# Optimization experiments

Measured on AMD Instinct MI355X. Metric: run time of the kernel, lower is better.

Reference implementation:

```python
import jax, jax.numpy as jnp
import numpy as np

A = 2
IMG_C = 3
IMG_H = 64
IMG_W = 96
N_OBJ = 5   # OBJS + STACKS with REMOVE_BG
B = 64
P = 4       # number of predicate nets
CONV_OUT = 32


def setup_inputs() -> dict:
    key = jax.random.key(0)
    k0, k1, k2, k3 = jax.random.split(key, 4)
    state = jax.random.normal(k0, (B, N_OBJ, IMG_C, IMG_H, IMG_W), jnp.float32)
    state_next = jax.random.normal(k1, (B, N_OBJ, IMG_C, IMG_H, IMG_W), jnp.float32)
    # uniform object count (structural max N=5) so tuple count is static
    n_obj = jnp.full((B,), N_OBJ, dtype=jnp.int32)
    temp = jnp.float32(0.5)
    # stacked params for the P predicate nets (conv + linear head)
    conv_w = jax.random.normal(k2, (P * CONV_OUT, A * IMG_C, 3, 3), jnp.float32) * 0.05
    conv_b = jnp.zeros((P * CONV_OUT,), jnp.float32)
    w2 = jax.random.normal(k3, (P, CONV_OUT), jnp.float32) * 0.1
    b2 = jnp.zeros((P,), jnp.float32)
    return {"state": state, "state_next": state_next, "conv_w": conv_w,
            "conv_b": conv_b, "w2": w2, "b2": b2, "n_obj": n_obj, "temp": temp}


def _build_tuples(s, n):
    # cartesian_prod(arange(n), arange(n)) -> ordered pairs (i, j)
    ii = jnp.repeat(jnp.arange(n), n)   # [n*n]
    jj = jnp.tile(jnp.arange(n), n)     # [n*n]
    a = s[:, ii]                        # [B, n*n, C, H, W]
    b = s[:, jj]
    t = jnp.concatenate([a, b], axis=2)             # [B, n*n, A*C, H, W]
    return t.reshape(-1, A * IMG_C, IMG_H, IMG_W)   # [B*n*n, 6, H, W]


def _predicates(t, conv_w, conv_b, w2, b2, temp):
    # fused conv over all P nets (stacked output channels)
    y = jax.lax.conv_general_dilated(
        t, conv_w, window_strides=(2, 2), padding='SAME',
        dimension_numbers=('NCHW', 'OIHW', 'NCHW'))
    y = jax.nn.relu(y + conv_b[None, :, None, None])
    y = y.mean(axis=(2, 3)).reshape(-1, P, CONV_OUT)   # [T, P, 32]
    logits = jnp.einsum('tpc,pc->tp', y, w2) + b2      # [T, P]
    return jax.nn.sigmoid(logits / temp)


def reference(state, state_next, conv_w, conv_b, w2, b2, n_obj, temp):
    n = N_OBJ  # uniform ragged case: all n_obj entries equal the max
    tuples = _build_tuples(state, n)
    tuples_next = _build_tuples(state_next, n)
    preds = _predicates(tuples, conv_w, conv_b, w2, b2, temp)
    preds_next = _predicates(tuples_next, conv_w, conv_b, w2, b2, temp)
    # adjacency: column per tuple, one-hot in the owning sample's row
    T = B * n * n
    adj = (jnp.arange(T)[None, :] // (n * n) == jnp.arange(B)[:, None]).astype(jnp.float32)
    return preds, preds_next, adj
```

## Files before the change

### kernel.cpp

```cpp
#include <hip/hip_runtime.h>
#include <math.h>

#define BQ 64
#define NOBJ 5
#define CIN 3
#define IMG_H 64
#define IMG_W 96
#define OH 32
#define OW 48
#define NPAIR 25
#define PP 4
#define CONV_OUT 32

#define NRG 16
#define NPOS 96
#define XK 32
#define X_U32 (NOBJ * NPOS * XK / 2)
#define X_UNITS (NOBJ * NPOS * 4)

#define NPRED (2 * 1600 * PP)
#define ADJ_N (BQ * 1600)

typedef __fp16   h2 __attribute__((ext_vector_type(2)));
typedef _Float16 half8 __attribute__((ext_vector_type(8)));
typedef float    float4_ __attribute__((ext_vector_type(4)));
typedef unsigned int uint4_ __attribute__((ext_vector_type(4)));

__global__ __launch_bounds__(512) void conv_pair_mfma(
    const float* __restrict__ state,
    const float* __restrict__ state_next,
    const float* __restrict__ conv_w,
    const float* __restrict__ conv_b,
    const float* __restrict__ w2,
    float* __restrict__ T,
    float* __restrict__ out)
{
    __shared__ __align__(16) unsigned int sX32[X_U32];

    const int tid = threadIdx.x;
    const int rg  = blockIdx.x;
    const int b   = blockIdx.y;
    const int src = blockIdx.z;

    const float* g = (src == 0 ? state : state_next)
                   + (size_t)b * NOBJ * CIN * IMG_H * IMG_W;
    const int R0 = rg * 4;

    if (src == 1 && tid < 100) {
        int a  = (rg + NRG * b) * 100 + tid;
        int bb = a / 1600;
        int t  = a - bb * 1600;
        out[NPRED + a] = (t / NPAIR == bb) ? 1.0f : 0.0f;
    }

    const int wave = tid >> 6;
    const int lane = tid & 63;
    const int quad = lane >> 4;
    const int ocl  = lane & 15;

    const int mt  = wave;
    const int p   = mt >> 1;
    const int row = mt * 16 + ocl;

    half8 wa, wb;
    #pragma unroll
    for (int j = 0; j < 8; ++j) {
        int k = quad * 8 + j;
        float va = 0.f, vb = 0.f;
        if (k < 27) {
            va = conv_w[row * 54 + k];
            vb = conv_w[row * 54 + 27 + k];
        } else if (k == 27) {
            va = conv_b[row];
        }
        wa[j] = (_Float16)va;
        wb[j] = (_Float16)vb;
    }
    h2 w2h01, w2h23;
    {
        const float* wp = w2 + p * CONV_OUT + (mt & 1) * 16 + quad * 4;
        w2h01 = __builtin_amdgcn_cvt_pkrtz(wp[0], wp[1]);
        w2h23 = __builtin_amdgcn_cvt_pkrtz(wp[2], wp[3]);
    }

    {
        const int subk = tid & 3;
        int koff[8], khv[8], kwv[8];
        float padf[8];
        bool kval[8];
        #pragma unroll
        for (int j = 0; j < 8; ++j) {
            int k = subk * 8 + j;
            if (k < 27) {
                int ci = k / 9;
                int r9 = k - ci * 9;
                int kh = r9 / 3;
                int kw = r9 - kh * 3;
                koff[j] = ci * (IMG_H * IMG_W) + kh * IMG_W + kw;
                khv[j] = kh; kwv[j] = kw; kval[j] = true; padf[j] = 0.f;
            } else {
                koff[j] = 0; khv[j] = 0; kwv[j] = 0; kval[j] = false;
                padf[j] = (k == 27) ? 1.0f : 0.f;
            }
        }
        for (int u = tid; u < X_UNITS; u += 512) {
            int pl  = (u >> 2) % NPOS;
            int obj = u / (NPOS * 4);
            int rl  = (pl >= 48) ? 1 : 0;
            int pc  = pl - rl * 48;
            int gr0 = R0 + 2 * rl;
            int gc0 = 2 * pc;
            const float* gp = g + obj * (CIN * IMG_H * IMG_W) + gr0 * IMG_W + gc0;
            float fv[8];
            #pragma unroll
            for (int j = 0; j < 8; ++j) {
                float v = padf[j];
                if (kval[j] && (gr0 + khv[j] < IMG_H) && (gc0 + kwv[j] < IMG_W))
                    v = gp[koff[j]];
                fv[j] = v;
            }
            uint4_ w4;
            w4.x = __builtin_bit_cast(unsigned int, __builtin_amdgcn_cvt_pkrtz(fv[0], fv[1]));
            w4.y = __builtin_bit_cast(unsigned int, __builtin_amdgcn_cvt_pkrtz(fv[2], fv[3]));
            w4.z = __builtin_bit_cast(unsigned int, __builtin_amdgcn_cvt_pkrtz(fv[4], fv[5]));
            w4.w = __builtin_bit_cast(unsigned int, __builtin_amdgcn_cvt_pkrtz(fv[6], fv[7]));
            *(uint4_*)&sX32[(size_t)u * 4] = w4;
        }
    }

    __syncthreads();

    const float4_ zero4 = {0.f, 0.f, 0.f, 0.f};
    const h2 hz = {(__fp16)0.f, (__fp16)0.f};

    float acc[NPAIR];
    #pragma unroll
    for (int q = 0; q < NPAIR; ++q) acc[q] = 0.f;

    #pragma unroll
    for (int nt = 0; nt < 6; ++nt) {
        const int rl  = nt / 3;
        const int c0  = (nt - rl * 3) * 16;
        const int pos = rl * 48 + c0 + ocl;

        half8 xf[NOBJ];
        h2 ah01[NOBJ], ah23[NOBJ];
        #pragma unroll
        for (int obj = 0; obj < NOBJ; ++obj) {
            xf[obj] = *(const half8*)&sX32[((size_t)(obj * NPOS + pos)) * 16 + quad * 4];
            float4_ a = __builtin_amdgcn_mfma_f32_16x16x32_f16(wa, xf[obj], zero4, 0, 0, 0);
            ah01[obj] = __builtin_amdgcn_cvt_pkrtz(a[0], a[1]);
            ah23[obj] = __builtin_amdgcn_cvt_pkrtz(a[2], a[3]);
        }

        #pragma unroll
        for (int jo = 0; jo < NOBJ; ++jo) {
            float4_ bq = __builtin_amdgcn_mfma_f32_16x16x32_f16(wb, xf[jo], zero4, 0, 0, 0);
            h2 bh01 = __builtin_amdgcn_cvt_pkrtz(bq[0], bq[1]);
            h2 bh23 = __builtin_amdgcn_cvt_pkrtz(bq[2], bq[3]);
            #pragma unroll
            for (int i = 0; i < NOBJ; ++i) {
                h2 s0 = ah01[i] + bh01;
                h2 s1 = ah23[i] + bh23;
                s0 = __builtin_elementwise_max(s0, hz);
                s1 = __builtin_elementwise_max(s1, hz);
                float t0 = __builtin_amdgcn_fdot2(s0, w2h01, acc[i * NOBJ + jo], false);
                acc[i * NOBJ + jo] = __builtin_amdgcn_fdot2(s1, w2h23, t0, false);
            }
        }
    }

    float myv = 0.f;
    #pragma unroll
    for (int q = 0; q < NPAIR; ++q) {
        float rr = acc[q];
        #pragma unroll
        for (int off = 32; off > 0; off >>= 1)
            rr += __shfl_xor(rr, off, 64);
        if (lane == q) myv = rr;
    }
    if (lane < NPAIR)
        T[((((size_t)src * BQ + b) * NRG + rg) * NPAIR + lane) * 8 + mt] = myv;
}

__global__ __launch_bounds__(256) void pred_kernel(
    const float* __restrict__ T,
    const float* __restrict__ b2,
    const float* __restrict__ temp,
    float* __restrict__ out)
{
    int idx = blockIdx.x * blockDim.x + threadIdx.x;
    if (idx >= NPRED) return;
    int p   = idx & 3;
    int t   = (idx >> 2) % 1600;
    int src = idx / 6400;
    int bb  = t / NPAIR;
    int pr  = t - bb * NPAIR;
    const float* base = T + ((((size_t)src * BQ + bb) * NRG) * NPAIR + pr) * 8 + 2 * p;
    float sum = 0.f;
    #pragma unroll
    for (int rgi = 0; rgi < NRG; ++rgi) {
        sum += base[(size_t)rgi * NPAIR * 8];
        sum += base[(size_t)rgi * NPAIR * 8 + 1];
    }
    float logit = sum * (1.0f / (OH * OW)) + b2[p];
    float x = logit / temp[0];
    out[idx] = 1.0f / (1.0f + expf(-x));
}

extern "C" void kernel_launch(void* const* d_in, const int* in_sizes, int n_in,
                              void* d_out, int out_size, void* d_ws, size_t ws_size,
                              hipStream_t stream)
{
    const float* state      = (const float*)d_in[0];
    const float* state_next = (const float*)d_in[1];
    const float* conv_w     = (const float*)d_in[2];
    const float* conv_b     = (const float*)d_in[3];
    const float* w2         = (const float*)d_in[4];
    const float* b2         = (const float*)d_in[5];
    const float* temp       = (const float*)d_in[7];

    float* out = (float*)d_out;
    float* T   = (float*)d_ws;

    dim3 grid1(NRG, BQ, 2);
    conv_pair_mfma<<<grid1, 512, 0, stream>>>(state, state_next, conv_w, conv_b,
                                              w2, T, out);

    pred_kernel<<<(NPRED + 255) / 256, 256, 0, stream>>>(T, b2, temp, out);
}
```

Baseline: 152.9 us.

## Fuse predicate epilogue into conv kernel via last-block atomic counter

```diff
diff --git a/kernel.cpp b/kernel.cpp
--- a/kernel.cpp
+++ b/kernel.cpp
@@ -20,11 +20,30 @@
 
 #define NPRED (2 * 1600 * PP)
 #define ADJ_N (BQ * 1600)
+#define NBLOCKS (2 * BQ * NRG)
+
+#define CTR_OFFSET 2097152
 
 typedef __fp16   h2 __attribute__((ext_vector_type(2)));
 typedef _Float16 half8 __attribute__((ext_vector_type(8)));
 typedef float    float4_ __attribute__((ext_vector_type(4)));
 typedef unsigned int uint4_ __attribute__((ext_vector_type(4)));
+
+template<int CTRL, int RM>
+__device__ __forceinline__ float dpp_add(float x) {
+    int s = __builtin_amdgcn_update_dpp(0, __builtin_bit_cast(int, x),
+                                        CTRL, RM, 0xf, true);
+    return x + __builtin_bit_cast(float, s);
+}
+__device__ __forceinline__ float wave_sum64(float x) {
+    x = dpp_add<0x111, 0xf>(x);
+    x = dpp_add<0x112, 0xf>(x);
+    x = dpp_add<0x114, 0xf>(x);
+    x = dpp_add<0x118, 0xf>(x);
+    x = dpp_add<0x142, 0xa>(x);
+    x = dpp_add<0x143, 0xc>(x);
+    return x;
+}
 
 __global__ __launch_bounds__(512) void conv_pair_mfma(
     const float* __restrict__ state,
@@ -32,10 +51,14 @@
     const float* __restrict__ conv_w,
     const float* __restrict__ conv_b,
     const float* __restrict__ w2,
+    const float* __restrict__ b2,
+    const float* __restrict__ temp,
     float* __restrict__ T,
+    unsigned int* __restrict__ counter,
     float* __restrict__ out)
 {
     __shared__ __align__(16) unsigned int sX32[X_U32];
+    __shared__ int sLast;
 
     const int tid = threadIdx.x;
     const int rg  = blockIdx.x;
@@ -170,42 +193,45 @@
         }
     }
 
-    float myv = 0.f;
-    #pragma unroll
-    for (int q = 0; q < NPAIR; ++q) {
-        float rr = acc[q];
-        #pragma unroll
-        for (int off = 32; off > 0; off >>= 1)
-            rr += __shfl_xor(rr, off, 64);
-        if (lane == q) myv = rr;
-    }
-    if (lane < NPAIR)
-        T[((((size_t)src * BQ + b) * NRG + rg) * NPAIR + lane) * 8 + mt] = myv;
-}
-
-__global__ __launch_bounds__(256) void pred_kernel(
-    const float* __restrict__ T,
-    const float* __restrict__ b2,
-    const float* __restrict__ temp,
-    float* __restrict__ out)
-{
-    int idx = blockIdx.x * blockDim.x + threadIdx.x;
-    if (idx >= NPRED) return;
-    int p   = idx & 3;
-    int t   = (idx >> 2) % 1600;
-    int src = idx / 6400;
-    int bb  = t / NPAIR;
-    int pr  = t - bb * NPAIR;
-    const float* base = T + ((((size_t)src * BQ + bb) * NRG) * NPAIR + pr) * 8 + 2 * p;
-    float sum = 0.f;
-    #pragma unroll
-    for (int rgi = 0; rgi < NRG; ++rgi) {
-        sum += base[(size_t)rgi * NPAIR * 8];
-        sum += base[(size_t)rgi * NPAIR * 8 + 1];
-    }
-    float logit = sum * (1.0f / (OH * OW)) + b2[p];
-    float x = logit / temp[0];
-    out[idx] = 1.0f / (1.0f + expf(-x));
+    {
+        float* tp = T + ((((size_t)src * BQ + b) * NRG + rg) * NPAIR) * 8 + mt;
+        #pragma unroll
+        for (int q = 0; q < NPAIR; ++q) {
+            float rr = wave_sum64(acc[q]);
+            if (lane == 63) tp[q * 8] = rr;
+        }
+    }
+
+    __syncthreads();
+    if (tid == 0) {
+        __threadfence();
+        unsigned int old = atomicAdd(counter, 1u);
+        sLast = (old == (unsigned int)(NBLOCKS - 1)) ? 1 : 0;
+    }
+    __syncthreads();
+    if (sLast) {
+        __threadfence();
+        const float inv_temp = 1.0f / temp[0];
+        #pragma unroll
+        for (int i = 0; i < NPRED / 512; ++i) {
+            int idx  = tid + 512 * i;
+            int pp   = idx & 3;
+            int t    = (idx >> 2) % 1600;
+            int srci = idx / 6400;
+            int bb   = t / NPAIR;
+            int pr   = t - bb * NPAIR;
+            const float* base = T + ((((size_t)srci * BQ + bb) * NRG) * NPAIR + pr) * 8 + 2 * pp;
+            float sum = 0.f;
+            #pragma unroll
+            for (int rgi = 0; rgi < NRG; ++rgi) {
+                sum += base[(size_t)rgi * NPAIR * 8];
+                sum += base[(size_t)rgi * NPAIR * 8 + 1];
+            }
+            float logit = sum * (1.0f / (OH * OW)) + b2[pp];
+            float x = logit * inv_temp;
+            out[idx] = 1.0f / (1.0f + expf(-x));
+        }
+    }
 }
 
 extern "C" void kernel_launch(void* const* d_in, const int* in_sizes, int n_in,
@@ -222,10 +248,11 @@
 
     float* out = (float*)d_out;
     float* T   = (float*)d_ws;
+    unsigned int* counter = (unsigned int*)((char*)d_ws + CTR_OFFSET);
+
+    hipMemsetAsync(counter, 0, sizeof(unsigned int), stream);
 
     dim3 grid1(NRG, BQ, 2);
     conv_pair_mfma<<<grid1, 512, 0, stream>>>(state, state_next, conv_w, conv_b,
-                                              w2, T, out);
-
-    pred_kernel<<<(NPRED + 255) / 256, 256, 0, stream>>>(T, b2, temp, out);
-}
+                                              w2, b2, temp, T, counter, out);
+}
```

Measured after the change: 247.1 us. +61.6%, slower.
